# Optimization experiments

Measured on AMD Instinct MI355X. Metric: run time of the kernel, lower is better.

## Reference

```python
import jax, jax.numpy as jnp
import numpy as np

SEQ_LEN, PRED_LEN, PATCH_LEN, STRIDE, NUM_LAYERS = 512, 96, 16, 4, 2
NUM_QUBITS = 4
NUM_PATCHES = (SEQ_LEN - PATCH_LEN) // STRIDE + 1  # 125


def setup_inputs() -> dict:
    key = jax.random.key(0)
    k1, k2, k3, k4 = jax.random.split(key, 4)
    x = jax.random.normal(k1, (64, SEQ_LEN, 64), dtype=jnp.float32)
    weights = jax.random.uniform(k2, (NUM_LAYERS, NUM_QUBITS, 3), dtype=jnp.float32) * (2 * np.pi)
    head_w = jax.random.normal(k3, (PRED_LEN, NUM_PATCHES * NUM_QUBITS), dtype=jnp.float32) * 0.04
    head_b = jax.random.normal(k4, (PRED_LEN,), dtype=jnp.float32) * 0.01
    return {"x": x, "weights": weights, "head_w": head_w, "head_b": head_b}


def _apply_rot(state, phi, theta, omega, wire):
    # Rot = RZ(omega) RY(theta) RZ(phi); PennyLane wire 0 is MSB -> tensor axis wire+1
    c = jnp.cos(0.5 * theta)
    s = jnp.sin(0.5 * theta)
    e = lambda a: jnp.exp(1j * a)
    half, diff = 0.5 * (phi + omega), 0.5 * (phi - omega)
    U = jnp.stack([jnp.stack([e(-half) * c, -e(diff) * s]),
                   jnp.stack([e(-diff) * s, e(half) * c])]).astype(jnp.complex64)  # [2,2]
    st = jnp.moveaxis(state, wire + 1, -1)
    st = st @ U.T  # new_j = sum_k U[j,k] old_k
    return jnp.moveaxis(st, -1, wire + 1)


def _cnot(state, c, t):
    # flip target axis where control bit == 1
    mshape = [1, 1, 1, 1, 1]
    mshape[c + 1] = 2
    mask = (jnp.arange(2) == 1).reshape(mshape)
    return jnp.where(mask, jnp.flip(state, axis=t + 1), state)


def _quantum_encoder(patches, weights):
    # patches: [N,16] real; AmplitudeEmbedding(normalize=True)
    psi = patches / jnp.linalg.norm(patches, axis=-1, keepdims=True)
    state = psi.astype(jnp.complex64).reshape(-1, 2, 2, 2, 2)  # [N,2,2,2,2], wire0=MSB
    for l in range(NUM_LAYERS):
        for q in range(NUM_QUBITS):
            state = _apply_rot(state, weights[l, q, 0], weights[l, q, 1], weights[l, q, 2], q)
        r = (l % (NUM_QUBITS - 1)) + 1  # default StronglyEntanglingLayers ranges
        for i in range(NUM_QUBITS):
            state = _cnot(state, i, (i + r) % NUM_QUBITS)
    probs = jnp.abs(state.reshape(-1, 16)) ** 2  # [N,16]
    # <Z_q> = sum_k p_k * (1 - 2*bit_q(k)), wire0 = MSB of 4-bit index
    bits = (np.arange(16)[:, None] >> (NUM_QUBITS - 1 - np.arange(NUM_QUBITS))[None, :]) & 1
    signs = jnp.asarray(1.0 - 2.0 * bits, dtype=jnp.float32)  # [16,4]
    return probs @ signs  # [N,4]


def reference(x, weights, head_w, head_b):
    B, L, M = x.shape
    xs = jnp.transpose(x, (0, 2, 1)).reshape(B * M, L)
    idx = np.arange(NUM_PATCHES)[:, None] * STRIDE + np.arange(PATCH_LEN)[None, :]
    xp = xs[:, idx].reshape(-1, PATCH_LEN) + 1e-6  # [B*M*NP, 16]
    enc = _quantum_encoder(xp, weights)  # [B*M*NP, 4]
    enc = enc.reshape(B * M, NUM_PATCHES * NUM_QUBITS)
    out = enc @ head_w.T + head_b  # [B*M, pred_len]
    return jnp.transpose(out.reshape(B, M, PRED_LEN), (0, 2, 1))
```

## Files before the change

kernel.cpp:

```cpp
#include <hip/hip_runtime.h>
#include <cmath>

#define BATCH 64
#define SEQLEN 512
#define NFEAT 64
#define NPATCH 125
#define PREDLEN 96
#define NCOLS 500

#define MG 8
#define XROW 528
#define ELD 520

typedef __attribute__((ext_vector_type(8))) short short8;
typedef __attribute__((ext_vector_type(4))) short short4v;
typedef __attribute__((ext_vector_type(4))) float f32x4;

__device__ __forceinline__ unsigned short f2bf(float f) {
    unsigned int u = __float_as_uint(f);
    u += 0x7FFFu + ((u >> 16) & 1u);
    return (unsigned short)(u >> 16);
}
__device__ __forceinline__ float bf2f(unsigned short h) {
    return __uint_as_float(((unsigned int)h) << 16);
}

__global__ __launch_bounds__(512) void qml_one(
    const float* __restrict__ x,
    const float* __restrict__ w,
    const float* __restrict__ hw,
    const float* __restrict__ hb,
    float* __restrict__ out)
{
    __shared__ float G[32 * 16];
    __shared__ unsigned short xh[MG][XROW];
    __shared__ unsigned short xl[MG][XROW];
    __shared__ unsigned short enc[MG][ELD];

    const int tid  = threadIdx.x;
    const int lane = tid & 63;
    const int lr   = lane & 15;
    const int kg   = lane >> 4;
    const int wv   = tid >> 6;
    const int b    = blockIdx.x >> 3;
    const int m0   = (blockIdx.x & 7) * MG;

    if (wv == 0) {
        float my[8];
        {
            const int  g     = lane & 7;
            const float phi   = w[g * 3 + 0];
            const float theta = w[g * 3 + 1];
            const float omega = w[g * 3 + 2];
            const float c  = cosf(0.5f * theta), s  = sinf(0.5f * theta);
            const float hf = 0.5f * (phi + omega), df = 0.5f * (phi - omega);
            const float ch = cosf(hf), sh = sinf(hf);
            const float cd = cosf(df), sd = sinf(df);
            my[0] =  ch * c;  my[1] = -sh * c;
            my[2] = -cd * s;  my[3] = -sd * s;
            my[4] =  cd * s;  my[5] = -sd * s;
            my[6] =  ch * c;  my[7] =  sh * c;
        }
        float re[16], im[16];
        #pragma unroll
        for (int k = 0; k < 16; ++k) { re[k] = (k == (lane & 15)) ? 1.f : 0.f; im[k] = 0.f; }
        #pragma unroll
        for (int l = 0; l < 2; ++l) {
            #pragma unroll
            for (int qq = 0; qq < 4; ++qq) {
                const int g = l * 4 + qq;
                const float u00r = __shfl(my[0], g), u00i = __shfl(my[1], g);
                const float u01r = __shfl(my[2], g), u01i = __shfl(my[3], g);
                const float u10r = __shfl(my[4], g), u10i = __shfl(my[5], g);
                const float u11r = __shfl(my[6], g), u11i = __shfl(my[7], g);
                const int bit = 8 >> qq;
                #pragma unroll
                for (int k = 0; k < 16; ++k) {
                    if (k & bit) continue;
                    const int k1 = k | bit;
                    const float a0r = re[k],  a0i = im[k];
                    const float a1r = re[k1], a1i = im[k1];
                    re[k]  = u00r * a0r - u00i * a0i + u01r * a1r - u01i * a1i;
                    im[k]  = u00r * a0i + u00i * a0r + u01r * a1i + u01i * a1r;
                    re[k1] = u10r * a0r - u10i * a0i + u11r * a1r - u11i * a1i;
                    im[k1] = u10r * a0i + u10i * a0r + u11r * a1i + u11i * a1r;
                }
            }
            const int r = (l % 3) + 1;
            #pragma unroll
            for (int i = 0; i < 4; ++i) {
                const int cb = 8 >> i;
                const int tb = 8 >> ((i + r) & 3);
                #pragma unroll
                for (int k = 0; k < 16; ++k) {
                    if ((k & cb) && !(k & tb)) {
                        const int k1 = k | tb;
                        float t;
                        t = re[k]; re[k] = re[k1]; re[k1] = t;
                        t = im[k]; im[k] = im[k1]; im[k1] = t;
                    }
                }
            }
        }
        if (lane < 16) {
            #pragma unroll
            for (int k = 0; k < 16; ++k) {
                G[k * 16 + lane]        = re[k];
                G[(16 + k) * 16 + lane] = im[k];
            }
        }
    } else {
        const float* xb = x + (size_t)b * SEQLEN * NFEAT + m0;
        for (int idx = tid - 64; idx < XROW * 2; idx += 448) {
            const int t    = idx >> 1;
            const int half = idx & 1;
            float4 v = (t < SEQLEN)
                ? *reinterpret_cast<const float4*>(xb + (size_t)t * NFEAT + 4 * half)
                : make_float4(0.f, 0.f, 0.f, 0.f);
            const float vals[4] = {v.x, v.y, v.z, v.w};
            #pragma unroll
            for (int c = 0; c < 4; ++c) {
                const float vv = vals[c] + 1e-6f;
                const unsigned short h = f2bf(vv);
                xh[4 * half + c][t] = h;
                xl[4 * half + c][t] = f2bf(vv - bf2f(h));
            }
        }
    }
    __syncthreads();

    short8 ah0, al0, ah1, al1;
    {
        const int koff = (kg & 1) * 8;
        #pragma unroll
        for (int c = 0; c < 8; ++c) {
            const float g0 = G[lr * 16 + koff + c];
            const unsigned short h0 = f2bf(g0);
            ah0[c] = (short)h0;
            al0[c] = (short)f2bf(g0 - bf2f(h0));
            const float g1 = G[(16 + lr) * 16 + koff + c];
            const unsigned short h1 = f2bf(g1);
            ah1[c] = (short)h1;
            al1[c] = (short)f2bf(g1 - bf2f(h1));
        }
    }

    {
        const int m = wv;
        const unsigned short* xrow = (kg < 2) ? &xh[m][0] : &xl[m][0];
        #pragma unroll 1
        for (int nt = 0; nt < 8; ++nt) {
            const int p = nt * 16 + lr;

            const short4v* src = reinterpret_cast<const short4v*>(xrow + 4 * p + (kg & 1) * 8);
            const short4v s0 = src[0];
            const short4v s1 = src[1];
            short8 bfrag;
            #pragma unroll
            for (int c = 0; c < 4; ++c) { bfrag[c] = s0[c]; bfrag[c + 4] = s1[c]; }

            const f32x4 zz = {0.f, 0.f, 0.f, 0.f};
            f32x4 acc0 = __builtin_amdgcn_mfma_f32_16x16x32_bf16(al0, bfrag, zz, 0, 0, 0);
            acc0 = __builtin_amdgcn_mfma_f32_16x16x32_bf16(ah0, bfrag, acc0, 0, 0, 0);
            f32x4 acc1 = __builtin_amdgcn_mfma_f32_16x16x32_bf16(al1, bfrag, zz, 0, 0, 0);
            acc1 = __builtin_amdgcn_mfma_f32_16x16x32_bf16(ah1, bfrag, acc1, 0, 0, 0);

            const float p0 = acc0[0] * acc0[0] + acc1[0] * acc1[0];
            const float p1 = acc0[1] * acc0[1] + acc1[1] * acc1[1];
            const float p2 = acc0[2] * acc0[2] + acc1[2] * acc1[2];
            const float p3 = acc0[3] * acc0[3] + acc1[3] * acc1[3];
            const float psum = (p0 + p1) + (p2 + p3);
            float s0v = (kg & 2) ? psum : 0.f;
            float s1v = (kg & 1) ? psum : 0.f;
            float s2v = p2 + p3;
            float s3v = p1 + p3;
            float sav = psum;
            s0v += __shfl_xor(s0v, 16); s0v += __shfl_xor(s0v, 32);
            s1v += __shfl_xor(s1v, 16); s1v += __shfl_xor(s1v, 32);
            s2v += __shfl_xor(s2v, 16); s2v += __shfl_xor(s2v, 32);
            s3v += __shfl_xor(s3v, 16); s3v += __shfl_xor(s3v, 32);
            sav += __shfl_xor(sav, 16); sav += __shfl_xor(sav, 32);

            const float rinv = 1.f / sav;
            const float ssel = (kg == 0) ? s0v : (kg == 1) ? s1v : (kg == 2) ? s2v : s3v;
            const float zval = 1.f - 2.f * ssel * rinv;
            enc[m][4 * p + kg] = (p < NPATCH) ? f2bf(zval) : (unsigned short)0;
        }
    }
    __syncthreads();

    if (wv < 6) {
        const int o = wv * 16 + lr;
        const float* hwrow = hw + (size_t)o * NCOLS;
        const unsigned short* erow = &enc[lr & 7][0];

        f32x4 acc = {0.f, 0.f, 0.f, 0.f};
        #pragma unroll 2
        for (int kc = 0; kc < 15; ++kc) {
            const int k0 = kc * 32 + kg * 8;
            const short8 e = *reinterpret_cast<const short8*>(erow + k0);
            const float4 w0 = *reinterpret_cast<const float4*>(hwrow + k0);
            const float4 w1 = *reinterpret_cast<const float4*>(hwrow + k0 + 4);
            short8 wf;
            wf[0] = (short)f2bf(w0.x); wf[1] = (short)f2bf(w0.y);
            wf[2] = (short)f2bf(w0.z); wf[3] = (short)f2bf(w0.w);
            wf[4] = (short)f2bf(w1.x); wf[5] = (short)f2bf(w1.y);
            wf[6] = (short)f2bf(w1.z); wf[7] = (short)f2bf(w1.w);
            acc = __builtin_amdgcn_mfma_f32_16x16x32_bf16(e, wf, acc, 0, 0, 0);
        }
        {
            const int k0 = 480 + kg * 8;
            const short8 e = *reinterpret_cast<const short8*>(erow + k0);
            short8 wf;
            #pragma unroll
            for (int c = 0; c < 8; ++c) {
                const int k = k0 + c;
                wf[c] = (k < NCOLS) ? (short)f2bf(hwrow[k]) : (short)0;
            }
            acc = __builtin_amdgcn_mfma_f32_16x16x32_bf16(e, wf, acc, 0, 0, 0);
        }

        if (kg < 2) {
            const float bias = hb[o];
            #pragma unroll
            for (int j = 0; j < 4; ++j) {
                const int m = m0 + 4 * kg + j;
                out[((size_t)b * PREDLEN + o) * NFEAT + m] = acc[j] + bias;
            }
        }
    }
}

extern "C" void kernel_launch(void* const* d_in, const int* in_sizes, int n_in,
                              void* d_out, int out_size, void* d_ws, size_t ws_size,
                              hipStream_t stream) {
    const float* x  = (const float*)d_in[0];
    const float* w  = (const float*)d_in[1];
    const float* hw = (const float*)d_in[2];
    const float* hb = (const float*)d_in[3];
    float* out = (float*)d_out;

    (void)d_ws; (void)ws_size; (void)in_sizes; (void)n_in; (void)out_size;
    qml_one<<<dim3(BATCH * MG), dim3(512), 0, stream>>>(x, w, hw, hb, out);
}
```

Before: 28.41 us.

## Halve features per block, double grid, use packed bf16 conversion

Each block now handles 4 features instead of 8, with 256 threads, so the grid doubles to 1024 blocks. The head GEMM loops its 6 output tiles over 4 waves. Per-element bf16 rounding of the head weights is replaced with the packed v_cvt_pk_bf16_f32 instruction. The goal is better occupancy and less conversion ALU work. In exchange, the quantum gate matrix is recomputed in twice as many blocks, head_w is reloaded per block, and the 16-row MFMA tile is now only a quarter used.

```diff
diff --git a/kernel.cpp b/kernel.cpp
--- a/kernel.cpp
+++ b/kernel.cpp
@@ -8,7 +8,7 @@
 #define PREDLEN 96
 #define NCOLS 500
 
-#define MG 8
+#define MG 4
 #define XROW 528
 #define ELD 520
 
@@ -24,8 +24,13 @@
 __device__ __forceinline__ float bf2f(unsigned short h) {
     return __uint_as_float(((unsigned int)h) << 16);
 }
-
-__global__ __launch_bounds__(512) void qml_one(
+__device__ __forceinline__ unsigned int cvtpk(float lo, float hi) {
+    unsigned int r;
+    asm volatile("v_cvt_pk_bf16_f32 %0, %1, %2" : "=v"(r) : "v"(lo), "v"(hi));
+    return r;
+}
+
+__global__ __launch_bounds__(256) void qml_one(
     const float* __restrict__ x,
     const float* __restrict__ w,
     const float* __restrict__ hw,
@@ -42,13 +47,13 @@
     const int lr   = lane & 15;
     const int kg   = lane >> 4;
     const int wv   = tid >> 6;
-    const int b    = blockIdx.x >> 3;
-    const int m0   = (blockIdx.x & 7) * MG;
+    const int b    = blockIdx.x >> 4;
+    const int m0   = (blockIdx.x & 15) * MG;
 
     if (wv == 0) {
         float my[8];
         {
-            const int  g     = lane & 7;
+            const int  g      = lane & 7;
             const float phi   = w[g * 3 + 0];
             const float theta = w[g * 3 + 1];
             const float omega = w[g * 3 + 2];
@@ -111,19 +116,17 @@
         }
     } else {
         const float* xb = x + (size_t)b * SEQLEN * NFEAT + m0;
-        for (int idx = tid - 64; idx < XROW * 2; idx += 448) {
-            const int t    = idx >> 1;
-            const int half = idx & 1;
+        for (int t = tid - 64; t < XROW; t += 192) {
             float4 v = (t < SEQLEN)
-                ? *reinterpret_cast<const float4*>(xb + (size_t)t * NFEAT + 4 * half)
+                ? *reinterpret_cast<const float4*>(xb + (size_t)t * NFEAT)
                 : make_float4(0.f, 0.f, 0.f, 0.f);
             const float vals[4] = {v.x, v.y, v.z, v.w};
             #pragma unroll
             for (int c = 0; c < 4; ++c) {
                 const float vv = vals[c] + 1e-6f;
                 const unsigned short h = f2bf(vv);
-                xh[4 * half + c][t] = h;
-                xl[4 * half + c][t] = f2bf(vv - bf2f(h));
+                xh[c][t] = h;
+                xl[c][t] = f2bf(vv - bf2f(h));
             }
         }
     }
@@ -189,24 +192,25 @@
     }
     __syncthreads();
 
-    if (wv < 6) {
-        const int o = wv * 16 + lr;
+    const unsigned short* erow = &enc[lr & 3][0];
+    #pragma unroll 1
+    for (int t = wv; t < 6; t += 4) {
+        const int o = t * 16 + lr;
         const float* hwrow = hw + (size_t)o * NCOLS;
-        const unsigned short* erow = &enc[lr & 7][0];
 
         f32x4 acc = {0.f, 0.f, 0.f, 0.f};
         #pragma unroll 2
         for (int kc = 0; kc < 15; ++kc) {
             const int k0 = kc * 32 + kg * 8;
-            const short8 e = *reinterpret_cast<const short8*>(erow + k0);
+            const short8 e  = *reinterpret_cast<const short8*>(erow + k0);
             const float4 w0 = *reinterpret_cast<const float4*>(hwrow + k0);
             const float4 w1 = *reinterpret_cast<const float4*>(hwrow + k0 + 4);
-            short8 wf;
-            wf[0] = (short)f2bf(w0.x); wf[1] = (short)f2bf(w0.y);
-            wf[2] = (short)f2bf(w0.z); wf[3] = (short)f2bf(w0.w);
-            wf[4] = (short)f2bf(w1.x); wf[5] = (short)f2bf(w1.y);
-            wf[6] = (short)f2bf(w1.z); wf[7] = (short)f2bf(w1.w);
-            acc = __builtin_amdgcn_mfma_f32_16x16x32_bf16(e, wf, acc, 0, 0, 0);
+            union { unsigned int u[4]; short8 s; } wf;
+            wf.u[0] = cvtpk(w0.x, w0.y);
+            wf.u[1] = cvtpk(w0.z, w0.w);
+            wf.u[2] = cvtpk(w1.x, w1.y);
+            wf.u[3] = cvtpk(w1.z, w1.w);
+            acc = __builtin_amdgcn_mfma_f32_16x16x32_bf16(e, wf.s, acc, 0, 0, 0);
         }
         {
             const int k0 = 480 + kg * 8;
@@ -220,11 +224,11 @@
             acc = __builtin_amdgcn_mfma_f32_16x16x32_bf16(e, wf, acc, 0, 0, 0);
         }
 
-        if (kg < 2) {
+        if (kg == 0) {
             const float bias = hb[o];
             #pragma unroll
             for (int j = 0; j < 4; ++j) {
-                const int m = m0 + 4 * kg + j;
+                const int m = m0 + j;
                 out[((size_t)b * PREDLEN + o) * NFEAT + m] = acc[j] + bias;
             }
         }
@@ -241,5 +245,5 @@
     float* out = (float*)d_out;
 
     (void)d_ws; (void)ws_size; (void)in_sizes; (void)n_in; (void)out_size;
-    qml_one<<<dim3(BATCH * MG), dim3(512), 0, stream>>>(x, w, hw, hb, out);
-}
+    qml_one<<<dim3(BATCH * (NFEAT / MG)), dim3(256), 0, stream>>>(x, w, hw, hb, out);
+}
```

Result: slower. 38.11 us (+34.1%).
